# Optimization experiments

Measured on AMD Instinct MI355X. Metric: run time of the kernel, lower is better.

Reference implementation:

```python
import jax, jax.numpy as jnp
import numpy as np

EPS = 1e-6
MAX_Q = 25.0
B, M, N, S = 1024, 8192, 32, 128


def setup_inputs() -> dict:
    key = jax.random.key(0)
    k = jax.random.split(key, 6)
    z = jax.random.normal(k[0], (B, N), jnp.float32) * 1e-3
    z_j = jax.random.uniform(k[1], (M, N), jnp.float32, -1e-3, 1e-3)
    vec_d_j = jax.random.uniform(k[2], (M, N), jnp.float32, -1e-3, 1e-3)
    T_hat_j = jax.random.uniform(k[3], (M, S), jnp.float32, -1e-3, 1e-3)
    alpha_j = jnp.ones((M,), jnp.float32)
    sigma_par = jax.random.uniform(k[4], (M,), jnp.float32, 0.9, 1.5)
    sigma_perp = jax.random.uniform(k[5], (M,), jnp.float32, 0.1, 0.8)
    return {"z": z, "z_j": z_j, "vec_d_j": vec_d_j, "T_hat_j": T_hat_j,
            "alpha_j": alpha_j, "sigma_par": sigma_par, "sigma_perp": sigma_perp}


def reference(z, z_j, vec_d_j, T_hat_j, alpha_j, sigma_par, sigma_perp):
    tiny = jnp.finfo(sigma_par.dtype).eps
    w_par = 1.0 / jnp.maximum(sigma_par, tiny) ** 2      # [M]
    w_perp = 1.0 / jnp.maximum(sigma_perp, tiny) ** 2    # [M]
    w_diff = w_par - w_perp                               # [M]

    dz = z[:, None, :] - z_j[None, :, :]                  # [B, M, N]
    dz_norm_sq = jnp.sum(dz * dz, axis=-1)                # [B, M]

    d_norm = jnp.linalg.norm(vec_d_j, axis=-1, keepdims=True)  # [M, 1]
    use_proj = (d_norm > EPS).astype(z.dtype)                   # [M, 1]
    b = jnp.where(d_norm > EPS, vec_d_j / d_norm, jnp.zeros_like(vec_d_j))  # [M, N]
    proj = jnp.einsum('bmn,mn->bm', dz, b) * use_proj[:, 0][None, :]        # [B, M]

    q_pos = w_perp[None, :] * dz_norm_sq + w_diff[None, :] * (proj * proj)  # [B, M]
    q_pos = jnp.minimum(q_pos, jnp.asarray(MAX_Q, dtype=z.dtype))

    gain = alpha_j[None, :] * jnp.exp(-jnp.pi * q_pos)    # [B, M]
    T = gain @ T_hat_j                                     # [B, S]
    return T
```

## Files before the change

kernel.cpp:

```cpp
#include <hip/hip_runtime.h>
#include <hip/hip_bf16.h>
#include <math.h>

#define B_SZ 1024
#define M_SZ 8192
#define N_SZ 32
#define S_SZ 128

#define MT   256
#define BT   64
#define NTHR 256
#define NSPLIT 32

#define SG_STRIDE 264

typedef __bf16 bf16x8 __attribute__((ext_vector_type(8)));
typedef float  f32x4  __attribute__((ext_vector_type(4)));

#define WS_TSWZ   ((size_t)0)
#define WS_ZJBF   ((size_t)2 * 1024 * 1024)
#define WS_DVBF   (WS_ZJBF + (size_t)M_SZ * N_SZ * 2)
#define WS_MCONST (WS_DVBF + (size_t)M_SZ * N_SZ * 2)
#define WS_ZBF    (WS_MCONST + (size_t)M_SZ * 8 * 4)
#define WS_ZN     (WS_ZBF + (size_t)B_SZ * N_SZ * 2)
#define WS_PART   ((size_t)4 * 1024 * 1024)
#define WS_NEED   (WS_PART + (size_t)NSPLIT * B_SZ * S_SZ * 4)

__global__ __launch_bounds__(256)
void prep_kernel(const float* __restrict__ T,
                 const float* __restrict__ z,
                 const float* __restrict__ zj_in,
                 const float* __restrict__ dv_in,
                 const float* __restrict__ alpha_j,
                 const float* __restrict__ sigma_par,
                 const float* __restrict__ sigma_perp,
                 char* __restrict__ ws)
{
    const int bx = blockIdx.x;
    const int t  = threadIdx.x;

    if (bx < 512) {
        const int g    = bx * 256 + t;
        const int mc   = g >> 9;
        const int ns   = (g >> 6) & 7;
        const int lane = g & 63;
        const int c    = lane & 15;
        const int q    = lane >> 4;
        const float* src = T + (size_t)(mc * 32 + q * 8) * S_SZ + ns * 16 + c;
        bf16x8 v;
        #pragma unroll
        for (int j = 0; j < 8; ++j) v[j] = (__bf16)src[(size_t)j * S_SZ];
        *(bf16x8*)(ws + WS_TSWZ + (size_t)g * 16) = v;
    } else if (bx < 544) {
        const int m = (bx - 512) * 256 + t;
        float a[N_SZ], d[N_SZ];
        const float4* a4 = (const float4*)(zj_in + (size_t)m * N_SZ);
        const float4* d4 = (const float4*)(dv_in + (size_t)m * N_SZ);
        #pragma unroll
        for (int i = 0; i < N_SZ / 4; ++i) {
            float4 av = a4[i], dw = d4[i];
            a[4*i+0]=av.x; a[4*i+1]=av.y; a[4*i+2]=av.z; a[4*i+3]=av.w;
            d[4*i+0]=dw.x; d[4*i+1]=dw.y; d[4*i+2]=dw.z; d[4*i+3]=dw.w;
        }
        float zjn = 0.f, dnsq = 0.f, zjd = 0.f;
        #pragma unroll
        for (int n = 0; n < N_SZ; ++n) {
            zjn += a[n]*a[n]; dnsq += d[n]*d[n]; zjd += a[n]*d[n];
        }
        const float dn  = sqrtf(dnsq);
        const float inv = (dn > 1e-6f) ? (1.0f / dn) : 0.0f;
        __bf16* zjb = (__bf16*)(ws + WS_ZJBF) + (size_t)m * N_SZ;
        __bf16* dvb = (__bf16*)(ws + WS_DVBF) + (size_t)m * N_SZ;
        #pragma unroll
        for (int i = 0; i < 4; ++i) {
            bf16x8 vz, vd;
            #pragma unroll
            for (int j = 0; j < 8; ++j) {
                vz[j] = (__bf16)a[i*8+j];
                vd[j] = (__bf16)(d[i*8+j] * inv);
            }
            *(bf16x8*)(zjb + i*8) = vz;
            *(bf16x8*)(dvb + i*8) = vd;
        }
        const float tiny = 1.1920928955078125e-07f;
        const float sp  = fmaxf(sigma_par[m],  tiny);
        const float spp = fmaxf(sigma_perp[m], tiny);
        const float wperp = 1.0f / (spp * spp);
        const float wdiff = 1.0f / (sp * sp) - wperp;
        float* mc8 = (float*)(ws + WS_MCONST) + (size_t)m * 8;
        *(f32x4*)mc8       = (f32x4){wperp, wperp * zjn, wdiff, zjd * inv};
        *(f32x4*)(mc8 + 4) = (f32x4){alpha_j[m], 0.f, 0.f, 0.f};
    } else {
        const int b = (bx - 544) * 256 + t;
        float v[N_SZ];
        const float4* z4 = (const float4*)(z + (size_t)b * N_SZ);
        #pragma unroll
        for (int i = 0; i < N_SZ / 4; ++i) {
            float4 w4 = z4[i];
            v[4*i+0]=w4.x; v[4*i+1]=w4.y; v[4*i+2]=w4.z; v[4*i+3]=w4.w;
        }
        float zn = 0.f;
        #pragma unroll
        for (int n = 0; n < N_SZ; ++n) zn += v[n]*v[n];
        __bf16* zb = (__bf16*)(ws + WS_ZBF) + (size_t)b * N_SZ;
        #pragma unroll
        for (int i = 0; i < 4; ++i) {
            bf16x8 vz;
            #pragma unroll
            for (int j = 0; j < 8; ++j) vz[j] = (__bf16)v[i*8+j];
            *(bf16x8*)(zb + i*8) = vz;
        }
        ((float*)(ws + WS_ZN))[b] = zn;
    }
}

__global__ __launch_bounds__(NTHR, 4)
void cpsf_main_kernel(const char* __restrict__ ws_ro, float* __restrict__ ws_part)
{
    __shared__ __align__(16) __bf16 sG[BT * SG_STRIDE];

    const int t     = threadIdx.x;
    const int lane  = t & 63;
    const int w     = t >> 6;
    const int q     = lane >> 4;
    const int c     = lane & 15;
    const int mx    = blockIdx.x;
    const int m0    = mx * MT;
    const int bbase = blockIdx.y * BT;

    const __bf16* zbf   = (const __bf16*)(ws_ro + WS_ZBF);
    const __bf16* zjbf  = (const __bf16*)(ws_ro + WS_ZJBF);
    const __bf16* dvbf  = (const __bf16*)(ws_ro + WS_DVBF);
    const float*  mcst  = (const float*)(ws_ro + WS_MCONST);
    const float*  znp   = (const float*)(ws_ro + WS_ZN);
    const char*   Tswz  = ws_ro + WS_TSWZ;

    const bf16x8 zA  = *(const bf16x8*)(zbf + ((size_t)(bbase + w*16 + c) * N_SZ + q*8));
    const f32x4  zn4 = *(const f32x4*)(znp + bbase + w*16 + q*4);

    const float PI_F = 3.14159274101257324f;
    #pragma unroll 4
    for (int tile = 0; tile < MT / 16; ++tile) {
        const size_t boff = (size_t)(m0 + tile*16 + c) * N_SZ + q*8;
        const bf16x8 bz = *(const bf16x8*)(zjbf + boff);
        const bf16x8 bd = *(const bf16x8*)(dvbf + boff);
        f32x4 s1 = __builtin_amdgcn_mfma_f32_16x16x32_bf16(zA, bz, (f32x4){0.f,0.f,0.f,0.f}, 0, 0, 0);
        f32x4 sd = __builtin_amdgcn_mfma_f32_16x16x32_bf16(zA, bd, (f32x4){0.f,0.f,0.f,0.f}, 0, 0, 0);
        const float* mc8 = mcst + (size_t)(m0 + tile*16 + c) * 8;
        const f32x4 mc0 = *(const f32x4*)mc8;
        const float al  = mc8[4];
        #pragma unroll
        for (int reg = 0; reg < 4; ++reg) {
            const float t1 = fmaf(s1[reg], -2.0f, zn4[reg]);
            float qv = fmaf(mc0[0], t1, mc0[1]);
            const float p  = sd[reg] - mc0[3];
            qv = fmaf(mc0[2] * p, p, qv);
            qv = fminf(qv, 25.0f);
            const float g = al * __expf(-PI_F * qv);
            sG[(size_t)(w*16 + q*4 + reg) * SG_STRIDE + tile*16 + c] = (__bf16)g;
        }
    }
    __syncthreads();

    f32x4 acc[4][2];
    #pragma unroll
    for (int bt = 0; bt < 4; ++bt)
        #pragma unroll
        for (int i = 0; i < 2; ++i) acc[bt][i] = (f32x4){0.f,0.f,0.f,0.f};

    #pragma unroll 2
    for (int kc = 0; kc < MT / 32; ++kc) {
        const int mc = mx * (MT / 32) + kc;
        bf16x8 bfr[2];
        #pragma unroll
        for (int i = 0; i < 2; ++i)
            bfr[i] = *(const bf16x8*)(Tswz + ((size_t)(mc*8 + w*2 + i) * 64 + lane) * 16);
        #pragma unroll
        for (int bt = 0; bt < 4; ++bt) {
            const bf16x8 a = *(const bf16x8*)((const char*)sG
                              + (size_t)(bt*16 + c) * (SG_STRIDE*2) + kc*64 + q*16);
            #pragma unroll
            for (int i = 0; i < 2; ++i)
                acc[bt][i] = __builtin_amdgcn_mfma_f32_16x16x32_bf16(a, bfr[i], acc[bt][i], 0, 0, 0);
        }
    }

    #pragma unroll
    for (int bt = 0; bt < 4; ++bt) {
        float* part = ws_part + (size_t)mx * (B_SZ * S_SZ)
                    + (size_t)(bbase + bt*16 + q*4) * S_SZ + w*32 + c;
        #pragma unroll
        for (int i = 0; i < 2; ++i)
            #pragma unroll
            for (int reg = 0; reg < 4; ++reg)
                part[(size_t)reg * S_SZ + i*16] = acc[bt][i][reg];
    }
}

__global__ __launch_bounds__(256)
void reduce_kernel(const float* __restrict__ part, float* __restrict__ out)
{
    const int i = blockIdx.x * 256 + threadIdx.x;
    const f32x4* p = (const f32x4*)part;
    f32x4 s = p[i];
    #pragma unroll
    for (int sp = 1; sp < NSPLIT; ++sp)
        s = s + p[(size_t)sp * (B_SZ * S_SZ / 4) + i];
    ((f32x4*)out)[i] = s;
}

#define SGF_STRIDE 68
__global__ __launch_bounds__(NTHR, 2)
void cpsf_fused_fallback(const float* __restrict__ z,
                         const float* __restrict__ z_j,
                         const float* __restrict__ vec_d_j,
                         const float* __restrict__ T_hat,
                         const float* __restrict__ alpha_j,
                         const float* __restrict__ sigma_par,
                         const float* __restrict__ sigma_perp,
                         float* __restrict__ out)
{
    __shared__ float sZ[BT * N_SZ];
    __shared__ float sZn[BT];
    __shared__ float sG[MT * SGF_STRIDE];

    const int t     = threadIdx.x;
    const int m0    = blockIdx.x * MT;
    const int bbase = blockIdx.y * BT;

    {
        const float4* z4 = (const float4*)z + (size_t)bbase * (N_SZ / 4);
        float4* s4 = (float4*)sZ;
        #pragma unroll
        for (int i = t; i < BT * N_SZ / 4; i += NTHR) s4[i] = z4[i];
    }
    const int m = m0 + t;
    float zj[N_SZ], dv[N_SZ];
    {
        const float4* a4 = (const float4*)(z_j     + (size_t)m * N_SZ);
        const float4* d4 = (const float4*)(vec_d_j + (size_t)m * N_SZ);
        #pragma unroll
        for (int i = 0; i < N_SZ / 4; ++i) {
            float4 av = a4[i], dw = d4[i];
            zj[4*i+0]=av.x; zj[4*i+1]=av.y; zj[4*i+2]=av.z; zj[4*i+3]=av.w;
            dv[4*i+0]=dw.x; dv[4*i+1]=dw.y; dv[4*i+2]=dw.z; dv[4*i+3]=dw.w;
        }
    }
    float zjn = 0.f, dnsq = 0.f, zjd = 0.f;
    #pragma unroll
    for (int n = 0; n < N_SZ; ++n) {
        zjn += zj[n]*zj[n]; dnsq += dv[n]*dv[n]; zjd += zj[n]*dv[n];
    }
    const float dn = sqrtf(dnsq);
    const float inv_dn = (dn > 1e-6f) ? (1.0f / dn) : 0.0f;
    const float P0 = zjd * inv_dn;
    const float tiny = 1.1920928955078125e-07f;
    const float sp  = fmaxf(sigma_par[m],  tiny);
    const float spp = fmaxf(sigma_perp[m], tiny);
    const float wperp = 1.0f / (spp * spp);
    const float wdiff = 1.0f / (sp * sp) - wperp;
    const float Cc = wperp * zjn;
    const float al = alpha_j[m];

    __syncthreads();
    if (t < BT) {
        float s = 0.f;
        #pragma unroll
        for (int n = 0; n < N_SZ; ++n) { float v = sZ[t*N_SZ+n]; s += v*v; }
        sZn[t] = s;
    }
    __syncthreads();

    const float PI_F = 3.14159274101257324f;
    for (int bq = 0; bq < BT / 4; ++bq) {
        float g[4];
        #pragma unroll
        for (int k = 0; k < 4; ++k) {
            const int b = bq*4 + k;
            float s1 = 0.f, sd = 0.f;
            #pragma unroll
            for (int n = 0; n < N_SZ; ++n) {
                const float zv = sZ[b*N_SZ+n];
                s1 += zv*zj[n]; sd += zv*dv[n];
            }
            const float p = sd*inv_dn - P0;
            float qv = wperp*sZn[b] - 2.0f*wperp*s1 + Cc + wdiff*p*p;
            qv = fminf(qv, 25.0f);
            g[k] = al * __expf(-PI_F*qv);
        }
        *(float4*)&sG[t*SGF_STRIDE + bq*4] = make_float4(g[0],g[1],g[2],g[3]);
    }
    __syncthreads();

    const int sg = t & 15, bg = t >> 4;
    const int b0 = bg*4, s0 = sg*8;
    float acc[4][8];
    #pragma unroll
    for (int i = 0; i < 4; ++i)
        #pragma unroll
        for (int j = 0; j < 8; ++j) acc[i][j] = 0.f;
    const float4* th4 = (const float4*)T_hat + (size_t)m0*(S_SZ/4) + sg*2;
    for (int mm = 0; mm < MT; ++mm) {
        const float4 g4 = *(const float4*)&sG[mm*SGF_STRIDE + b0];
        const float4 ta = th4[(size_t)mm*(S_SZ/4)];
        const float4 tb = th4[(size_t)mm*(S_SZ/4)+1];
        const float gg[4] = {g4.x,g4.y,g4.z,g4.w};
        const float tv[8] = {ta.x,ta.y,ta.z,ta.w,tb.x,tb.y,tb.z,tb.w};
        #pragma unroll
        for (int i = 0; i < 4; ++i)
            #pragma unroll
            for (int j = 0; j < 8; ++j) acc[i][j] += gg[i]*tv[j];
    }
    float* op = out + (size_t)(bbase + b0)*S_SZ + s0;
    #pragma unroll
    for (int i = 0; i < 4; ++i)
        #pragma unroll
        for (int j = 0; j < 8; ++j)
            unsafeAtomicAdd(&op[i*S_SZ + j], acc[i][j]);
}

extern "C" void kernel_launch(void* const* d_in, const int* in_sizes, int n_in,
                              void* d_out, int out_size, void* d_ws, size_t ws_size,
                              hipStream_t stream) {
    (void)in_sizes; (void)n_in; (void)out_size;

    const float* z          = (const float*)d_in[0];
    const float* z_j        = (const float*)d_in[1];
    const float* vec_d_j    = (const float*)d_in[2];
    const float* T_hat_j    = (const float*)d_in[3];
    const float* alpha_j    = (const float*)d_in[4];
    const float* sigma_par  = (const float*)d_in[5];
    const float* sigma_perp = (const float*)d_in[6];
    float* out = (float*)d_out;

    if (ws_size >= WS_NEED) {
        char*  ws   = (char*)d_ws;
        float* part = (float*)(ws + WS_PART);

        prep_kernel<<<dim3(548), 256, 0, stream>>>(
            T_hat_j, z, z_j, vec_d_j, alpha_j, sigma_par, sigma_perp, ws);

        dim3 grid(NSPLIT, B_SZ / BT);
        cpsf_main_kernel<<<grid, NTHR, 0, stream>>>(ws, part);

        reduce_kernel<<<dim3(B_SZ * S_SZ / (256 * 4)), 256, 0, stream>>>(part, out);
    } else {
        hipMemsetAsync(out, 0, (size_t)B_SZ * S_SZ * sizeof(float), stream);
        dim3 grid(M_SZ / MT, B_SZ / BT);
        cpsf_fused_fallback<<<grid, NTHR, 0, stream>>>(
            z, z_j, vec_d_j, T_hat_j, alpha_j, sigma_par, sigma_perp, out);
    }
}
```

Before: 94.95 us.

## Halve batch tile, split gain tiles across waves, fold pi into exp2 constants

The main kernel's batch tile drops from 64 to 32. Each block therefore covers fewer rows, the grid doubles, and each pair of waves shares the 16 M-tiles, so the per-wave gain-computation loop is halved. The pi*log2e factor is folded into the precomputed per-M constants so the gain becomes a single exp2 of a clamped exponent, removing a multiply. The reduce kernel now uses one scalar element per thread instead of vector-4 loads. The risk is that the doubled block count repeats the T_hat and z_j loads per block, and the scalar reduce issues narrower memory accesses.

```diff
diff --git a/kernel.cpp b/kernel.cpp
--- a/kernel.cpp
+++ b/kernel.cpp
@@ -8,7 +8,7 @@
 #define S_SZ 128
 
 #define MT   256
-#define BT   64
+#define BT   32
 #define NTHR 256
 #define NSPLIT 32
 
@@ -16,6 +16,19 @@
 
 typedef __bf16 bf16x8 __attribute__((ext_vector_type(8)));
 typedef float  f32x4  __attribute__((ext_vector_type(4)));
+
+#if defined(__has_builtin)
+#if __has_builtin(__builtin_amdgcn_exp2f)
+#define EXP2F(x) __builtin_amdgcn_exp2f(x)
+#else
+#define EXP2F(x) exp2f(x)
+#endif
+#else
+#define EXP2F(x) exp2f(x)
+#endif
+
+#define NEG_PI_LOG2E  (-4.5323601722717285f)
+#define E_CLAMP       (-113.30900573730469f)
 
 #define WS_TSWZ   ((size_t)0)
 #define WS_ZJBF   ((size_t)2 * 1024 * 1024)
@@ -87,8 +100,9 @@
         const float spp = fmaxf(sigma_perp[m], tiny);
         const float wperp = 1.0f / (spp * spp);
         const float wdiff = 1.0f / (sp * sp) - wperp;
+        const float A = NEG_PI_LOG2E * wperp;
         float* mc8 = (float*)(ws + WS_MCONST) + (size_t)m * 8;
-        *(f32x4*)mc8       = (f32x4){wperp, wperp * zjn, wdiff, zjd * inv};
+        *(f32x4*)mc8       = (f32x4){A, A * zjn, NEG_PI_LOG2E * wdiff, zjd * inv};
         *(f32x4*)(mc8 + 4) = (f32x4){alpha_j[m], 0.f, 0.f, 0.f};
     } else {
         const int b = (bx - 544) * 256 + t;
@@ -135,40 +149,43 @@
     const float*  znp   = (const float*)(ws_ro + WS_ZN);
     const char*   Tswz  = ws_ro + WS_TSWZ;
 
-    const bf16x8 zA  = *(const bf16x8*)(zbf + ((size_t)(bbase + w*16 + c) * N_SZ + q*8));
-    const f32x4  zn4 = *(const f32x4*)(znp + bbase + w*16 + q*4);
-
-    const float PI_F = 3.14159274101257324f;
+    const int wb  = w & 1;
+    const int mt0 = (w >> 1) * 8;
+
+    const bf16x8 zA  = *(const bf16x8*)(zbf + ((size_t)(bbase + wb*16 + c) * N_SZ + q*8));
+    const f32x4  zn4 = *(const f32x4*)(znp + bbase + wb*16 + q*4);
+
     #pragma unroll 4
-    for (int tile = 0; tile < MT / 16; ++tile) {
-        const size_t boff = (size_t)(m0 + tile*16 + c) * N_SZ + q*8;
-        const bf16x8 bz = *(const bf16x8*)(zjbf + boff);
-        const bf16x8 bd = *(const bf16x8*)(dvbf + boff);
+    for (int ti = 0; ti < 8; ++ti) {
+        const int tile = mt0 + ti;
+        const int mg   = m0 + tile*16 + c;
+        const bf16x8 bz = *(const bf16x8*)(zjbf + (size_t)mg * N_SZ + q*8);
+        const bf16x8 bd = *(const bf16x8*)(dvbf + (size_t)mg * N_SZ + q*8);
         f32x4 s1 = __builtin_amdgcn_mfma_f32_16x16x32_bf16(zA, bz, (f32x4){0.f,0.f,0.f,0.f}, 0, 0, 0);
         f32x4 sd = __builtin_amdgcn_mfma_f32_16x16x32_bf16(zA, bd, (f32x4){0.f,0.f,0.f,0.f}, 0, 0, 0);
-        const float* mc8 = mcst + (size_t)(m0 + tile*16 + c) * 8;
+        const float* mc8 = mcst + (size_t)mg * 8;
         const f32x4 mc0 = *(const f32x4*)mc8;
         const float al  = mc8[4];
         #pragma unroll
         for (int reg = 0; reg < 4; ++reg) {
             const float t1 = fmaf(s1[reg], -2.0f, zn4[reg]);
-            float qv = fmaf(mc0[0], t1, mc0[1]);
-            const float p  = sd[reg] - mc0[3];
-            qv = fmaf(mc0[2] * p, p, qv);
-            qv = fminf(qv, 25.0f);
-            const float g = al * __expf(-PI_F * qv);
-            sG[(size_t)(w*16 + q*4 + reg) * SG_STRIDE + tile*16 + c] = (__bf16)g;
+            float e = fmaf(mc0[0], t1, mc0[1]);
+            const float p = sd[reg] - mc0[3];
+            e = fmaf(mc0[2] * p, p, e);
+            e = fmaxf(e, E_CLAMP);
+            const float g = al * EXP2F(e);
+            sG[(size_t)(wb*16 + q*4 + reg) * SG_STRIDE + tile*16 + c] = (__bf16)g;
         }
     }
     __syncthreads();
 
-    f32x4 acc[4][2];
-    #pragma unroll
-    for (int bt = 0; bt < 4; ++bt)
+    f32x4 acc[2][2];
+    #pragma unroll
+    for (int bt = 0; bt < 2; ++bt)
         #pragma unroll
         for (int i = 0; i < 2; ++i) acc[bt][i] = (f32x4){0.f,0.f,0.f,0.f};
 
-    #pragma unroll 2
+    #pragma unroll
     for (int kc = 0; kc < MT / 32; ++kc) {
         const int mc = mx * (MT / 32) + kc;
         bf16x8 bfr[2];
@@ -176,7 +193,7 @@
         for (int i = 0; i < 2; ++i)
             bfr[i] = *(const bf16x8*)(Tswz + ((size_t)(mc*8 + w*2 + i) * 64 + lane) * 16);
         #pragma unroll
-        for (int bt = 0; bt < 4; ++bt) {
+        for (int bt = 0; bt < 2; ++bt) {
             const bf16x8 a = *(const bf16x8*)((const char*)sG
                               + (size_t)(bt*16 + c) * (SG_STRIDE*2) + kc*64 + q*16);
             #pragma unroll
@@ -186,7 +203,7 @@
     }
 
     #pragma unroll
-    for (int bt = 0; bt < 4; ++bt) {
+    for (int bt = 0; bt < 2; ++bt) {
         float* part = ws_part + (size_t)mx * (B_SZ * S_SZ)
                     + (size_t)(bbase + bt*16 + q*4) * S_SZ + w*32 + c;
         #pragma unroll
@@ -201,14 +218,15 @@
 void reduce_kernel(const float* __restrict__ part, float* __restrict__ out)
 {
     const int i = blockIdx.x * 256 + threadIdx.x;
-    const f32x4* p = (const f32x4*)part;
-    f32x4 s = p[i];
-    #pragma unroll
-    for (int sp = 1; sp < NSPLIT; ++sp)
-        s = s + p[(size_t)sp * (B_SZ * S_SZ / 4) + i];
-    ((f32x4*)out)[i] = s;
-}
-
+    float s = 0.f;
+    #pragma unroll 8
+    for (int sp = 0; sp < NSPLIT; ++sp)
+        s += part[(size_t)sp * (B_SZ * S_SZ) + i];
+    out[i] = s;
+}
+
+#define FB_MT 256
+#define FB_BT 64
 #define SGF_STRIDE 68
 __global__ __launch_bounds__(NTHR, 2)
 void cpsf_fused_fallback(const float* __restrict__ z,
@@ -220,19 +238,19 @@
                          const float* __restrict__ sigma_perp,
                          float* __restrict__ out)
 {
-    __shared__ float sZ[BT * N_SZ];
-    __shared__ float sZn[BT];
-    __shared__ float sG[MT * SGF_STRIDE];
+    __shared__ float sZ[FB_BT * N_SZ];
+    __shared__ float sZn[FB_BT];
+    __shared__ float sG[FB_MT * SGF_STRIDE];
 
     const int t     = threadIdx.x;
-    const int m0    = blockIdx.x * MT;
-    const int bbase = blockIdx.y * BT;
+    const int m0    = blockIdx.x * FB_MT;
+    const int bbase = blockIdx.y * FB_BT;
 
     {
         const float4* z4 = (const float4*)z + (size_t)bbase * (N_SZ / 4);
         float4* s4 = (float4*)sZ;
         #pragma unroll
-        for (int i = t; i < BT * N_SZ / 4; i += NTHR) s4[i] = z4[i];
+        for (int i = t; i < FB_BT * N_SZ / 4; i += NTHR) s4[i] = z4[i];
     }
     const int m = m0 + t;
     float zj[N_SZ], dv[N_SZ];
@@ -263,7 +281,7 @@
     const float al = alpha_j[m];
 
     __syncthreads();
-    if (t < BT) {
+    if (t < FB_BT) {
         float s = 0.f;
         #pragma unroll
         for (int n = 0; n < N_SZ; ++n) { float v = sZ[t*N_SZ+n]; s += v*v; }
@@ -272,7 +290,7 @@
     __syncthreads();
 
     const float PI_F = 3.14159274101257324f;
-    for (int bq = 0; bq < BT / 4; ++bq) {
+    for (int bq = 0; bq < FB_BT / 4; ++bq) {
         float g[4];
         #pragma unroll
         for (int k = 0; k < 4; ++k) {
@@ -300,7 +318,7 @@
         #pragma unroll
         for (int j = 0; j < 8; ++j) acc[i][j] = 0.f;
     const float4* th4 = (const float4*)T_hat + (size_t)m0*(S_SZ/4) + sg*2;
-    for (int mm = 0; mm < MT; ++mm) {
+    for (int mm = 0; mm < FB_MT; ++mm) {
         const float4 g4 = *(const float4*)&sG[mm*SGF_STRIDE + b0];
         const float4 ta = th4[(size_t)mm*(S_SZ/4)];
         const float4 tb = th4[(size_t)mm*(S_SZ/4)+1];
@@ -343,10 +361,10 @@
         dim3 grid(NSPLIT, B_SZ / BT);
         cpsf_main_kernel<<<grid, NTHR, 0, stream>>>(ws, part);
 
-        reduce_kernel<<<dim3(B_SZ * S_SZ / (256 * 4)), 256, 0, stream>>>(part, out);
+        reduce_kernel<<<dim3(B_SZ * S_SZ / 256), 256, 0, stream>>>(part, out);
     } else {
         hipMemsetAsync(out, 0, (size_t)B_SZ * S_SZ * sizeof(float), stream);
-        dim3 grid(M_SZ / MT, B_SZ / BT);
+        dim3 grid(M_SZ / FB_MT, B_SZ / FB_BT);
         cpsf_fused_fallback<<<grid, NTHR, 0, stream>>>(
             z, z_j, vec_d_j, T_hat_j, alpha_j, sigma_par, sigma_perp, out);
     }
```

Measured after the change: 96.37 us. No clear change (+1.5%).
